# Kernel optimization log

Measured on AMD Instinct MI355X. Metric: run time of the kernel, lower is better.

## Reference

```python
import jax, jax.numpy as jnp
import numpy as np

DIM = 512
HEADS = 8
DIM_HEAD = 64
INNER = HEADS * DIM_HEAD


def setup_inputs() -> dict:
    key = jax.random.key(0)
    k1, k2, k3, k4 = jax.random.split(key, 4)
    x = jax.random.normal(k1, (8, 2048, DIM), dtype=jnp.float32)
    # nn.Linear(dim, inner*3, bias=False): store as [dim, 3*inner] for x @ W
    w_qkv = jax.random.normal(k2, (DIM, 3 * INNER), dtype=jnp.float32) * (DIM ** -0.5)
    w_out = jax.random.normal(k3, (INNER, DIM), dtype=jnp.float32) * (INNER ** -0.5)
    b_out = jax.random.normal(k4, (DIM,), dtype=jnp.float32) * 0.01
    # learnable log-scale, init = log(dim_head**-0.5)
    log_scale = jnp.asarray(np.log(DIM_HEAD ** -0.5), dtype=jnp.float32)
    return {"x": x, "w_qkv": w_qkv, "w_out": w_out, "b_out": b_out, "log_scale": log_scale}


def reference(x, w_qkv, w_out, b_out, log_scale):
    b, n, _ = x.shape
    qkv = x @ w_qkv                                   # [b, n, 3*inner]
    q, k, v = jnp.split(qkv, 3, axis=-1)
    def to_heads(t):
        return t.reshape(b, n, HEADS, DIM_HEAD).transpose(0, 2, 1, 3)  # [b,h,n,d]
    q, k, v = to_heads(q), to_heads(k), to_heads(v)
    dots = jnp.einsum('bhid,bhjd->bhij', q, k) * jnp.exp(log_scale)    # [b,h,n,n]
    mask_value = -jnp.finfo(dots.dtype).max
    eye = jnp.eye(n, dtype=bool)
    dots = jnp.where(eye, mask_value, dots)           # exclude self token
    attn = jax.nn.softmax(dots, axis=-1)
    out = jnp.einsum('bhij,bhjd->bhid', attn, v)      # [b,h,n,d]
    out = out.transpose(0, 2, 1, 3).reshape(b, n, INNER)
    return out @ w_out + b_out
```

## Files before the change

kernel.cpp:

```cpp
#include <hip/hip_runtime.h>
#include <hip/hip_bf16.h>
#include <cstddef>

#define DIMK 512
#define HEADS 8
#define DHEAD 64
#define NSEQ 2048
#define NB 8
#define M_TOT (NB * NSEQ)

typedef __attribute__((ext_vector_type(8))) short bf16x8;
typedef __attribute__((ext_vector_type(4))) float f32x4;

__device__ __forceinline__ unsigned short f2bf(float f) {
    union { float f; unsigned int u; } v; v.f = f;
    unsigned int r = v.u + 0x7fffu + ((v.u >> 16) & 1u);
    return (unsigned short)(r >> 16);
}

__device__ __forceinline__ unsigned int pk_bf_trunc(float hi, float lo) {
    union { float f; unsigned int u; } a, b; a.f = hi; b.f = lo;
    return __builtin_amdgcn_perm(a.u, b.u, 0x07060302u);
}

__device__ __forceinline__ float fexp2(float x) {
#if __has_builtin(__builtin_amdgcn_exp2f)
    return __builtin_amdgcn_exp2f(x);
#else
    return __expf(x * 0.69314718056f);
#endif
}

__device__ __forceinline__ void glds16(const unsigned short* g, unsigned short* l) {
    __builtin_amdgcn_global_load_lds(
        (const __attribute__((address_space(1))) void*)g,
        (__attribute__((address_space(3))) void*)l, 16, 0, 0);
}

__global__ __launch_bounds__(256) void f32_to_bf16(
    const float* __restrict__ in, unsigned short* __restrict__ out)
{
    const size_t i = ((size_t)blockIdx.x * 256 + threadIdx.x) * 8;
    const float4 a = *(const float4*)(in + i);
    const float4 b = *(const float4*)(in + i + 4);
    bf16x8 o;
    o[0] = (short)f2bf(a.x); o[1] = (short)f2bf(a.y);
    o[2] = (short)f2bf(a.z); o[3] = (short)f2bf(a.w);
    o[4] = (short)f2bf(b.x); o[5] = (short)f2bf(b.y);
    o[6] = (short)f2bf(b.z); o[7] = (short)f2bf(b.w);
    *(bf16x8*)(out + i) = o;
}

__global__ __launch_bounds__(256) void transpose_w(
    const float* __restrict__ W, unsigned short* __restrict__ WT,
    int K, int N, const float* __restrict__ log_scale, int nscale)
{
    __shared__ float t[32][33];
    const int tx = threadIdx.x & 31, ty = threadIdx.x >> 5;
    const int k0 = blockIdx.y * 32, n0 = blockIdx.x * 32;
    #pragma unroll
    for (int s = 0; s < 32; s += 8)
        t[ty + s][tx] = W[(size_t)(k0 + ty + s) * N + n0 + tx];
    __syncthreads();
    float sc = 1.0f;
    if (n0 < nscale) sc = __expf(log_scale[0]) * 1.4426950408889634f;
    #pragma unroll
    for (int s = 0; s < 32; s += 8)
        WT[(size_t)(n0 + ty + s) * K + k0 + tx] = f2bf(t[tx][ty + s] * sc);
}

__global__ __launch_bounds__(256) void gemm_qkv_mfma(
    const unsigned short* __restrict__ Xb, const unsigned short* __restrict__ WT,
    unsigned short* __restrict__ Qb, unsigned short* __restrict__ Kb,
    unsigned short* __restrict__ VTb)
{
    __shared__ unsigned short As[128 * 32];
    __shared__ unsigned short Bs[128 * 32];
    const int tid = threadIdx.x, wave = tid >> 6, lane = tid & 63;
    const int l16 = lane & 15, quad = lane >> 4;
    const int m0 = blockIdx.y * 128, col0 = blockIdx.x * 128;
    const int wrow = wave >> 1, wcol = wave & 1;

    unsigned short* lA0 = As + (wave * 16) * 32;
    unsigned short* lA1 = As + (64 + wave * 16) * 32;
    unsigned short* lB0 = Bs + (wave * 16) * 32;
    unsigned short* lB1 = Bs + (64 + wave * 16) * 32;
    const unsigned short* gA = Xb + (size_t)(m0 + wave * 16 + (lane >> 2)) * DIMK + (lane & 3) * 8;
    const unsigned short* gB = WT + (size_t)(col0 + wave * 16 + (lane >> 2)) * DIMK + (lane & 3) * 8;

    f32x4 acc[4][4];
    #pragma unroll
    for (int i = 0; i < 4; ++i)
        #pragma unroll
        for (int j = 0; j < 4; ++j) acc[i][j] = (f32x4){0.f, 0.f, 0.f, 0.f};

    for (int k0 = 0; k0 < DIMK; k0 += 32) {
        __syncthreads();
        glds16(gA + k0, lA0);
        glds16(gA + (size_t)64 * DIMK + k0, lA1);
        glds16(gB + k0, lB0);
        glds16(gB + (size_t)64 * DIMK + k0, lB1);
        __syncthreads();
        bf16x8 af[4], bfr[4];
        #pragma unroll
        for (int i = 0; i < 4; ++i)
            af[i] = *(const bf16x8*)(As + (wrow * 64 + i * 16 + l16) * 32 + quad * 8);
        #pragma unroll
        for (int j = 0; j < 4; ++j)
            bfr[j] = *(const bf16x8*)(Bs + (wcol * 64 + j * 16 + l16) * 32 + quad * 8);
        #pragma unroll
        for (int i = 0; i < 4; ++i)
            #pragma unroll
            for (int j = 0; j < 4; ++j)
                acc[i][j] = __builtin_amdgcn_mfma_f32_16x16x32_bf16(af[i], bfr[j], acc[i][j], 0, 0, 0);
    }

    const int which = blockIdx.x >> 2;
    #pragma unroll
    for (int i = 0; i < 4; ++i) {
        #pragma unroll
        for (int r = 0; r < 4; ++r) {
            const int gr = m0 + wrow * 64 + i * 16 + quad * 4 + r;
            const int bb = gr >> 11, n = gr & 2047;
            #pragma unroll
            for (int j = 0; j < 4; ++j) {
                const int col = col0 + wcol * 64 + j * 16 + l16;
                const int w = col & 511, h = w >> 6, d = w & 63;
                const size_t bh = (size_t)(bb * HEADS + h);
                const unsigned short val = f2bf(acc[i][j][r]);
                if (which == 0)      Qb[(bh * NSEQ + n) * DHEAD + d] = val;
                else if (which == 1) Kb[(bh * NSEQ + n) * DHEAD + d] = val;
                else                 VTb[(bh * DHEAD + d) * NSEQ + n] = val;
            }
        }
    }
}

__global__ __launch_bounds__(256) void gemm_out_mfma(
    const unsigned short* __restrict__ Ab, const unsigned short* __restrict__ BT,
    const float* __restrict__ bias, float* __restrict__ C)
{
    __shared__ unsigned short As[128 * 32];
    __shared__ unsigned short Bs[128 * 32];
    const int tid = threadIdx.x, wave = tid >> 6, lane = tid & 63;
    const int l16 = lane & 15, quad = lane >> 4;
    const int m0 = blockIdx.y * 128, col0 = blockIdx.x * 128;
    const int wrow = wave >> 1, wcol = wave & 1;

    unsigned short* lA0 = As + (wave * 16) * 32;
    unsigned short* lA1 = As + (64 + wave * 16) * 32;
    unsigned short* lB0 = Bs + (wave * 16) * 32;
    unsigned short* lB1 = Bs + (64 + wave * 16) * 32;
    const unsigned short* gA = Ab + (size_t)(m0 + wave * 16 + (lane >> 2)) * DIMK + (lane & 3) * 8;
    const unsigned short* gB = BT + (size_t)(col0 + wave * 16 + (lane >> 2)) * DIMK + (lane & 3) * 8;

    f32x4 acc[4][4];
    #pragma unroll
    for (int i = 0; i < 4; ++i)
        #pragma unroll
        for (int j = 0; j < 4; ++j) acc[i][j] = (f32x4){0.f, 0.f, 0.f, 0.f};

    for (int k0 = 0; k0 < DIMK; k0 += 32) {
        __syncthreads();
        glds16(gA + k0, lA0);
        glds16(gA + (size_t)64 * DIMK + k0, lA1);
        glds16(gB + k0, lB0);
        glds16(gB + (size_t)64 * DIMK + k0, lB1);
        __syncthreads();
        bf16x8 af[4], bfr[4];
        #pragma unroll
        for (int i = 0; i < 4; ++i)
            af[i] = *(const bf16x8*)(As + (wrow * 64 + i * 16 + l16) * 32 + quad * 8);
        #pragma unroll
        for (int j = 0; j < 4; ++j)
            bfr[j] = *(const bf16x8*)(Bs + (wcol * 64 + j * 16 + l16) * 32 + quad * 8);
        #pragma unroll
        for (int i = 0; i < 4; ++i)
            #pragma unroll
            for (int j = 0; j < 4; ++j)
                acc[i][j] = __builtin_amdgcn_mfma_f32_16x16x32_bf16(af[i], bfr[j], acc[i][j], 0, 0, 0);
    }

    #pragma unroll
    for (int i = 0; i < 4; ++i) {
        #pragma unroll
        for (int r = 0; r < 4; ++r) {
            const int gr = m0 + wrow * 64 + i * 16 + quad * 4 + r;
            #pragma unroll
            for (int j = 0; j < 4; ++j) {
                const int col = col0 + wcol * 64 + j * 16 + l16;
                C[(size_t)gr * 512 + col] = acc[i][j][r] + bias[col];
            }
        }
    }
}

__global__ __launch_bounds__(256) void attn_mfma(
    const unsigned short* __restrict__ Qb, const unsigned short* __restrict__ Kb,
    const unsigned short* __restrict__ VTb, unsigned short* __restrict__ O)
{
    __shared__ unsigned short Ks0[2][32 * 32];
    __shared__ unsigned short Ks1[2][32 * 32];
    __shared__ unsigned short Vs[2][64 * 32];
    __shared__ __align__(16) unsigned short Pq[4][2][16][40];

    const int tid  = threadIdx.x;
    const int wave = tid >> 6;
    const int lane = tid & 63;
    const int l16  = lane & 15;
    const int quad = lane >> 4;
    const int bh   = blockIdx.y;
    const int q0   = blockIdx.x * 128;
    const int qwA  = q0 + wave * 16;
    const int qwB  = q0 + 64 + wave * 16;

    const unsigned short* Qg = Qb  + (size_t)bh * NSEQ * DHEAD;
    const unsigned short* Kg = Kb  + (size_t)bh * NSEQ * DHEAD;
    const unsigned short* Vg = VTb + (size_t)bh * DHEAD * NSEQ;

    const bf16x8 b_qA0 = *(const bf16x8*)(Qg + (size_t)(qwA + l16) * DHEAD + quad * 8);
    const bf16x8 b_qA1 = *(const bf16x8*)(Qg + (size_t)(qwA + l16) * DHEAD + 32 + quad * 8);
    const bf16x8 b_qB0 = *(const bf16x8*)(Qg + (size_t)(qwB + l16) * DHEAD + quad * 8);
    const bf16x8 b_qB1 = *(const bf16x8*)(Qg + (size_t)(qwB + l16) * DHEAD + 32 + quad * 8);

    bf16x8 a_ones;
    #pragma unroll
    for (int i = 0; i < 8; ++i) a_ones[i] = (short)0x3F80;

    const int r16 = lane >> 2;
    const int c8  = (lane & 3) * 8;
    const unsigned short* src0;
    const unsigned short* src1;
    size_t step;
    unsigned short* dA[2];
    unsigned short* dB[2];
    if (wave == 0) {
        src0 = Kg + (size_t)r16 * DHEAD + c8;           src1 = src0 + 16 * DHEAD;
        step = 32 * DHEAD;
        dA[0] = &Ks0[0][0];  dA[1] = &Ks0[1][0];
        dB[0] = &Ks0[0][512]; dB[1] = &Ks0[1][512];
    } else if (wave == 1) {
        src0 = Kg + (size_t)r16 * DHEAD + 32 + c8;      src1 = src0 + 16 * DHEAD;
        step = 32 * DHEAD;
        dA[0] = &Ks1[0][0];  dA[1] = &Ks1[1][0];
        dB[0] = &Ks1[0][512]; dB[1] = &Ks1[1][512];
    } else if (wave == 2) {
        src0 = Vg + (size_t)r16 * NSEQ + c8;            src1 = src0 + (size_t)16 * NSEQ;
        step = 32;
        dA[0] = &Vs[0][0];   dA[1] = &Vs[1][0];
        dB[0] = &Vs[0][512]; dB[1] = &Vs[1][512];
    } else {
        src0 = Vg + (size_t)(32 + r16) * NSEQ + c8;     src1 = src0 + (size_t)16 * NSEQ;
        step = 32;
        dA[0] = &Vs[0][1024]; dA[1] = &Vs[1][1024];
        dB[0] = &Vs[0][1536]; dB[1] = &Vs[1][1536];
    }

    f32x4 oA[4], oB[4], laccA, laccB;
    #pragma unroll
    for (int t = 0; t < 4; ++t) { oA[t] = (f32x4){0.f,0.f,0.f,0.f}; oB[t] = (f32x4){0.f,0.f,0.f,0.f}; }
    laccA = (f32x4){0.f,0.f,0.f,0.f};
    laccB = (f32x4){0.f,0.f,0.f,0.f};

    glds16(src0, dA[0]);
    glds16(src1, dB[0]);
    src0 += step; src1 += step;

    for (int it = 0; it < NSEQ / 32; ++it) {
        const int cur = it & 1;
        const int j0  = it * 32;
        __syncthreads();

        if (it < NSEQ / 32 - 1) {
            glds16(src0, dA[cur ^ 1]);
            glds16(src1, dB[cur ^ 1]);
            src0 += step; src1 += step;
        }

        float pA[2][4], pB[2][4];
        #pragma unroll
        for (int t = 0; t < 2; ++t) {
            const bf16x8 a0 = *(const bf16x8*)(&Ks0[cur][(t * 16 + l16) * 32 + quad * 8]);
            const bf16x8 a1 = *(const bf16x8*)(&Ks1[cur][(t * 16 + l16) * 32 + quad * 8]);
            f32x4 sA = (f32x4){0.f,0.f,0.f,0.f}, sB = (f32x4){0.f,0.f,0.f,0.f};
            sA = __builtin_amdgcn_mfma_f32_16x16x32_bf16(a0, b_qA0, sA, 0, 0, 0);
            sA = __builtin_amdgcn_mfma_f32_16x16x32_bf16(a1, b_qA1, sA, 0, 0, 0);
            sB = __builtin_amdgcn_mfma_f32_16x16x32_bf16(a0, b_qB0, sB, 0, 0, 0);
            sB = __builtin_amdgcn_mfma_f32_16x16x32_bf16(a1, b_qB1, sB, 0, 0, 0);
            #pragma unroll
            for (int r = 0; r < 4; ++r) { pA[t][r] = fexp2(sA[r]); pB[t][r] = fexp2(sB[r]); }
            if (j0 + 16 * t == qwA) {
                #pragma unroll
                for (int r = 0; r < 4; ++r) if (l16 == quad * 4 + r) pA[t][r] = 0.f;
            }
            if (j0 + 16 * t == qwB) {
                #pragma unroll
                for (int r = 0; r < 4; ++r) if (l16 == quad * 4 + r) pB[t][r] = 0.f;
            }
        }

        #pragma unroll
        for (int t = 0; t < 2; ++t) {
            uint2 wA, wB;
            wA.x = pk_bf_trunc(pA[t][1], pA[t][0]); wA.y = pk_bf_trunc(pA[t][3], pA[t][2]);
            wB.x = pk_bf_trunc(pB[t][1], pB[t][0]); wB.y = pk_bf_trunc(pB[t][3], pB[t][2]);
            *(uint2*)(&Pq[wave][0][l16][t * 16 + quad * 4]) = wA;
            *(uint2*)(&Pq[wave][1][l16][t * 16 + quad * 4]) = wB;
        }
        __builtin_amdgcn_wave_barrier();

        const bf16x8 b_pA = *(const bf16x8*)(&Pq[wave][0][l16][quad * 8]);
        const bf16x8 b_pB = *(const bf16x8*)(&Pq[wave][1][l16][quad * 8]);

        laccA = __builtin_amdgcn_mfma_f32_16x16x32_bf16(a_ones, b_pA, laccA, 0, 0, 0);
        laccB = __builtin_amdgcn_mfma_f32_16x16x32_bf16(a_ones, b_pB, laccB, 0, 0, 0);
        #pragma unroll
        for (int t = 0; t < 4; ++t) {
            const bf16x8 v = *(const bf16x8*)(&Vs[cur][(t * 16 + l16) * 32 + quad * 8]);
            oA[t] = __builtin_amdgcn_mfma_f32_16x16x32_bf16(v, b_pA, oA[t], 0, 0, 0);
            oB[t] = __builtin_amdgcn_mfma_f32_16x16x32_bf16(v, b_pB, oB[t], 0, 0, 0);
        }
    }

    const float invA = 1.0f / laccA[0];
    const float invB = 1.0f / laccB[0];
    const int bb = bh >> 3, h = bh & 7;
    {
        const int n = qwA + l16;
        unsigned short* Orow = O + ((size_t)(bb * NSEQ + n)) * 512 + h * 64;
        #pragma unroll
        for (int t = 0; t < 4; ++t) {
            ushort4 o4;
            o4.x = f2bf(oA[t][0] * invA); o4.y = f2bf(oA[t][1] * invA);
            o4.z = f2bf(oA[t][2] * invA); o4.w = f2bf(oA[t][3] * invA);
            *(ushort4*)(Orow + t * 16 + quad * 4) = o4;
        }
    }
    {
        const int n = qwB + l16;
        unsigned short* Orow = O + ((size_t)(bb * NSEQ + n)) * 512 + h * 64;
        #pragma unroll
        for (int t = 0; t < 4; ++t) {
            ushort4 o4;
            o4.x = f2bf(oB[t][0] * invB); o4.y = f2bf(oB[t][1] * invB);
            o4.z = f2bf(oB[t][2] * invB); o4.w = f2bf(oB[t][3] * invB);
            *(ushort4*)(Orow + t * 16 + quad * 4) = o4;
        }
    }
}

extern "C" void kernel_launch(void* const* d_in, const int* in_sizes, int n_in,
                              void* d_out, int out_size, void* d_ws, size_t ws_size,
                              hipStream_t stream) {
    const float* x         = (const float*)d_in[0];
    const float* w_qkv     = (const float*)d_in[1];
    const float* w_out     = (const float*)d_in[2];
    const float* b_out     = (const float*)d_in[3];
    const float* log_scale = (const float*)d_in[4];
    float* out = (float*)d_out;

    char* ws = (char*)d_ws;
    const size_t NQKV = (size_t)NB * HEADS * NSEQ * DHEAD;
    unsigned short* xb  = (unsigned short*)(ws);
    unsigned short* Qb  = (unsigned short*)(ws + 2 * NQKV);
    unsigned short* Kb  = (unsigned short*)(ws + 4 * NQKV);
    unsigned short* VTb = (unsigned short*)(ws + 6 * NQKV);
    unsigned short* Ofb = (unsigned short*)(ws + 8 * NQKV);
    unsigned short* WqT = (unsigned short*)(ws + 10 * NQKV);
    unsigned short* WoT = (unsigned short*)(ws + 10 * NQKV + 4 * 1024 * 1024);

    f32_to_bf16<<<M_TOT * DIMK / (256 * 8), 256, 0, stream>>>(x, xb);
    transpose_w<<<dim3(1536 / 32, 512 / 32), 256, 0, stream>>>(w_qkv, WqT, 512, 1536, log_scale, 512);
    transpose_w<<<dim3(512 / 32, 512 / 32), 256, 0, stream>>>(w_out, WoT, 512, 512, log_scale, 0);

    gemm_qkv_mfma<<<dim3(1536 / 128, M_TOT / 128), 256, 0, stream>>>(xb, WqT, Qb, Kb, VTb);

    attn_mfma<<<dim3(NSEQ / 128, NB * HEADS), 256, 0, stream>>>(Qb, Kb, VTb, Ofb);

    gemm_out_mfma<<<dim3(512 / 128, M_TOT / 128), 256, 0, stream>>>(Ofb, WoT, b_out, out);
}
```

Measured before the change: 265.4 us.

## Load V fragments directly from global, merge weight transposes, swap grid axes

The attention kernel no longer stages V tiles through shared memory. Each wave reads its V fragments straight from global memory (L2) each iteration, and only K is double-buffered with async LDS copies spread across all four waves. The two weight-transpose launches are merged into one kernel, and every GEMM and attention grid swaps its x and y axes, which changes block scheduling order and cache locality. Removing V staging frees LDS and synchronisation work, at the cost of exposed global-load latency inside the loop.

New measurement: 307.8 us. +16.0%, slower.

```diff
diff --git a/kernel.cpp b/kernel.cpp
--- a/kernel.cpp
+++ b/kernel.cpp
@@ -51,22 +51,29 @@
     *(bf16x8*)(out + i) = o;
 }
 
-__global__ __launch_bounds__(256) void transpose_w(
-    const float* __restrict__ W, unsigned short* __restrict__ WT,
-    int K, int N, const float* __restrict__ log_scale, int nscale)
+__global__ __launch_bounds__(256) void transpose_both(
+    const float* __restrict__ w_qkv, const float* __restrict__ w_out,
+    unsigned short* __restrict__ WqT, unsigned short* __restrict__ WoT,
+    const float* __restrict__ log_scale)
 {
     __shared__ float t[32][33];
     const int tx = threadIdx.x & 31, ty = threadIdx.x >> 5;
-    const int k0 = blockIdx.y * 32, n0 = blockIdx.x * 32;
+    const int k0 = blockIdx.y * 32;
+    const float* W; unsigned short* WT; int N, n0;
+    float sc = 1.0f;
+    if (blockIdx.x < 48) {
+        W = w_qkv; WT = WqT; N = 1536; n0 = blockIdx.x * 32;
+        if (n0 < 512) sc = __expf(log_scale[0]) * 1.4426950408889634f;
+    } else {
+        W = w_out; WT = WoT; N = 512; n0 = (blockIdx.x - 48) * 32;
+    }
     #pragma unroll
     for (int s = 0; s < 32; s += 8)
         t[ty + s][tx] = W[(size_t)(k0 + ty + s) * N + n0 + tx];
     __syncthreads();
-    float sc = 1.0f;
-    if (n0 < nscale) sc = __expf(log_scale[0]) * 1.4426950408889634f;
     #pragma unroll
     for (int s = 0; s < 32; s += 8)
-        WT[(size_t)(n0 + ty + s) * K + k0 + tx] = f2bf(t[tx][ty + s] * sc);
+        WT[(size_t)(n0 + ty + s) * DIMK + k0 + tx] = f2bf(t[tx][ty + s] * sc);
 }
 
 __global__ __launch_bounds__(256) void gemm_qkv_mfma(
@@ -78,7 +85,9 @@
     __shared__ unsigned short Bs[128 * 32];
     const int tid = threadIdx.x, wave = tid >> 6, lane = tid & 63;
     const int l16 = lane & 15, quad = lane >> 4;
-    const int m0 = blockIdx.y * 128, col0 = blockIdx.x * 128;
+    const int m0 = blockIdx.x * 128;
+    const int cb = blockIdx.y;
+    const int col0 = cb * 128;
     const int wrow = wave >> 1, wcol = wave & 1;
 
     unsigned short* lA0 = As + (wave * 16) * 32;
@@ -115,7 +124,7 @@
                 acc[i][j] = __builtin_amdgcn_mfma_f32_16x16x32_bf16(af[i], bfr[j], acc[i][j], 0, 0, 0);
     }
 
-    const int which = blockIdx.x >> 2;
+    const int which = cb >> 2;
     #pragma unroll
     for (int i = 0; i < 4; ++i) {
         #pragma unroll
@@ -144,7 +153,7 @@
     __shared__ unsigned short Bs[128 * 32];
     const int tid = threadIdx.x, wave = tid >> 6, lane = tid & 63;
     const int l16 = lane & 15, quad = lane >> 4;
-    const int m0 = blockIdx.y * 128, col0 = blockIdx.x * 128;
+    const int m0 = blockIdx.x * 128, col0 = blockIdx.y * 128;
     const int wrow = wave >> 1, wcol = wave & 1;
 
     unsigned short* lA0 = As + (wave * 16) * 32;
@@ -201,7 +210,6 @@
 {
     __shared__ unsigned short Ks0[2][32 * 32];
     __shared__ unsigned short Ks1[2][32 * 32];
-    __shared__ unsigned short Vs[2][64 * 32];
     __shared__ __align__(16) unsigned short Pq[4][2][16][40];
 
     const int tid  = threadIdx.x;
@@ -209,8 +217,8 @@
     const int lane = tid & 63;
     const int l16  = lane & 15;
     const int quad = lane >> 4;
-    const int bh   = blockIdx.y;
-    const int q0   = blockIdx.x * 128;
+    const int bh   = blockIdx.x;
+    const int q0   = blockIdx.y * 128;
     const int qwA  = q0 + wave * 16;
     const int qwB  = q0 + 64 + wave * 16;
 
@@ -227,34 +235,12 @@
     #pragma unroll
     for (int i = 0; i < 8; ++i) a_ones[i] = (short)0x3F80;
 
-    const int r16 = lane >> 2;
-    const int c8  = (lane & 3) * 8;
-    const unsigned short* src0;
-    const unsigned short* src1;
-    size_t step;
-    unsigned short* dA[2];
-    unsigned short* dB[2];
-    if (wave == 0) {
-        src0 = Kg + (size_t)r16 * DHEAD + c8;           src1 = src0 + 16 * DHEAD;
-        step = 32 * DHEAD;
-        dA[0] = &Ks0[0][0];  dA[1] = &Ks0[1][0];
-        dB[0] = &Ks0[0][512]; dB[1] = &Ks0[1][512];
-    } else if (wave == 1) {
-        src0 = Kg + (size_t)r16 * DHEAD + 32 + c8;      src1 = src0 + 16 * DHEAD;
-        step = 32 * DHEAD;
-        dA[0] = &Ks1[0][0];  dA[1] = &Ks1[1][0];
-        dB[0] = &Ks1[0][512]; dB[1] = &Ks1[1][512];
-    } else if (wave == 2) {
-        src0 = Vg + (size_t)r16 * NSEQ + c8;            src1 = src0 + (size_t)16 * NSEQ;
-        step = 32;
-        dA[0] = &Vs[0][0];   dA[1] = &Vs[1][0];
-        dB[0] = &Vs[0][512]; dB[1] = &Vs[1][512];
-    } else {
-        src0 = Vg + (size_t)(32 + r16) * NSEQ + c8;     src1 = src0 + (size_t)16 * NSEQ;
-        step = 32;
-        dA[0] = &Vs[0][1024]; dA[1] = &Vs[1][1024];
-        dB[0] = &Vs[0][1536]; dB[1] = &Vs[1][1536];
-    }
+    const int r16 = lane >> 2, c8 = (lane & 3) * 8;
+    const unsigned short* srcK =
+        Kg + (size_t)((wave & 1) * 16 + r16) * DHEAD + (wave >> 1) * 32 + c8;
+    unsigned short* dK[2];
+    dK[0] = ((wave >> 1) ? &Ks1[0][0] : &Ks0[0][0]) + (wave & 1) * 512;
+    dK[1] = ((wave >> 1) ? &Ks1[1][0] : &Ks0[1][0]) + (wave & 1) * 512;
 
     f32x4 oA[4], oB[4], laccA, laccB;
     #pragma unroll
@@ -262,9 +248,8 @@
     laccA = (f32x4){0.f,0.f,0.f,0.f};
     laccB = (f32x4){0.f,0.f,0.f,0.f};
 
-    glds16(src0, dA[0]);
-    glds16(src1, dB[0]);
-    src0 += step; src1 += step;
+    glds16(srcK, dK[0]);
+    srcK += (size_t)32 * DHEAD;
 
     for (int it = 0; it < NSEQ / 32; ++it) {
         const int cur = it & 1;
@@ -272,10 +257,14 @@
         __syncthreads();
 
         if (it < NSEQ / 32 - 1) {
-            glds16(src0, dA[cur ^ 1]);
-            glds16(src1, dB[cur ^ 1]);
-            src0 += step; src1 += step;
-        }
+            glds16(srcK, dK[cur ^ 1]);
+            srcK += (size_t)32 * DHEAD;
+        }
+
+        bf16x8 vfrag[4];
+        #pragma unroll
+        for (int t = 0; t < 4; ++t)
+            vfrag[t] = *(const bf16x8*)(Vg + (size_t)(t * 16 + l16) * NSEQ + j0 + quad * 8);
 
         float pA[2][4], pB[2][4];
         #pragma unroll
@@ -316,9 +305,8 @@
         laccB = __builtin_amdgcn_mfma_f32_16x16x32_bf16(a_ones, b_pB, laccB, 0, 0, 0);
         #pragma unroll
         for (int t = 0; t < 4; ++t) {
-            const bf16x8 v = *(const bf16x8*)(&Vs[cur][(t * 16 + l16) * 32 + quad * 8]);
-            oA[t] = __builtin_amdgcn_mfma_f32_16x16x32_bf16(v, b_pA, oA[t], 0, 0, 0);
-            oB[t] = __builtin_amdgcn_mfma_f32_16x16x32_bf16(v, b_pB, oB[t], 0, 0, 0);
+            oA[t] = __builtin_amdgcn_mfma_f32_16x16x32_bf16(vfrag[t], b_pA, oA[t], 0, 0, 0);
+            oB[t] = __builtin_amdgcn_mfma_f32_16x16x32_bf16(vfrag[t], b_pB, oB[t], 0, 0, 0);
         }
     }
 
@@ -370,12 +358,11 @@
     unsigned short* WoT = (unsigned short*)(ws + 10 * NQKV + 4 * 1024 * 1024);
 
     f32_to_bf16<<<M_TOT * DIMK / (256 * 8), 256, 0, stream>>>(x, xb);
-    transpose_w<<<dim3(1536 / 32, 512 / 32), 256, 0, stream>>>(w_qkv, WqT, 512, 1536, log_scale, 512);
-    transpose_w<<<dim3(512 / 32, 512 / 32), 256, 0, stream>>>(w_out, WoT, 512, 512, log_scale, 0);
-
-    gemm_qkv_mfma<<<dim3(1536 / 128, M_TOT / 128), 256, 0, stream>>>(xb, WqT, Qb, Kb, VTb);
-
-    attn_mfma<<<dim3(NSEQ / 128, NB * HEADS), 256, 0, stream>>>(Qb, Kb, VTb, Ofb);
-
-    gemm_out_mfma<<<dim3(512 / 128, M_TOT / 128), 256, 0, stream>>>(Ofb, WoT, b_out, out);
-}
+    transpose_both<<<dim3(64, 16), 256, 0, stream>>>(w_qkv, w_out, WqT, WoT, log_scale);
+
+    gemm_qkv_mfma<<<dim3(M_TOT / 128, 1536 / 128), 256, 0, stream>>>(xb, WqT, Qb, Kb, VTb);
+
+    attn_mfma<<<dim3(NB * HEADS, NSEQ / 128), 256, 0, stream>>>(Qb, Kb, VTb, Ofb);
+
+    gemm_out_mfma<<<dim3(M_TOT / 128, 512 / 128), 256, 0, stream>>>(Ofb, WoT, b_out, out);
+}
```
